# Optimization experiments

Hardware: AMD Instinct MI355X
Metric: run time of the kernel (lower is better)

The kernel has to match this reference:

```python
import jax, jax.numpy as jnp
import numpy as np

# dilation list from _make_freq_dialtion with bins_per_octave=48, n_bins=352,
# max_ratio=9, bin_delta=0: round(48*log2(r)) for r in 2..9
DILATIONS = [48, 76, 96, 111, 124, 135, 144, 152]
B, T, F = 4, 512, 352
CF, HD = 16, 128  # conv_features, hd_conv_features (== dilated_conv_feature)


def _conv(x, w, b, pad, dil=(1, 1)):
    # x: NCHW, w: OIHW; symmetric padding -> matches torch padding=(ph,pw) / 'same' for odd kernels
    y = jax.lax.conv_general_dilated(
        x, w, window_strides=(1, 1),
        padding=[(pad[0], pad[0]), (pad[1], pad[1])],
        rhs_dilation=dil,
        dimension_numbers=("NCHW", "OIHW", "NCHW"))
    return y + b[None, :, None, None]


def _inorm(x, eps=1e-5):
    # torch InstanceNorm2d (affine=False): normalize each (n,c) plane over HxW
    m = jnp.mean(x, axis=(2, 3), keepdims=True)
    v = jnp.var(x, axis=(2, 3), keepdims=True)
    return (x - m) * jax.lax.rsqrt(v + eps)


def setup_inputs() -> dict:
    key = jax.random.key(0)
    ks = jax.random.split(key, 24)

    def w(k, shape, fan_in):
        s = 1.0 / np.sqrt(fan_in)
        return jax.random.uniform(k, shape, jnp.float32, -s, s)

    inp = {}
    inp["cqt"] = jax.random.normal(ks[0], (B, 1, T, F), jnp.float32)
    # 7x7 conv stack
    inp["w0"] = w(ks[1], (CF, 1, 7, 7), 1 * 49);       inp["b0"] = w(ks[2], (CF,), 1 * 49)
    inp["w1"] = w(ks[3], (CF, CF, 7, 7), CF * 49);      inp["b1"] = w(ks[4], (CF,), CF * 49)
    inp["w2"] = w(ks[5], (CF, CF, 7, 7), CF * 49);      inp["b2"] = w(ks[6], (CF,), CF * 49)
    # stacked harmonic dilated convs (1x3), one per dilation
    inp["w_hd"] = w(ks[7], (len(DILATIONS), HD, CF, 1, 3), CF * 3)
    inp["b_hd"] = w(ks[8], (len(DILATIONS), HD), CF * 3)
    # d_cnn
    inp["wd0"] = w(ks[9], (HD, HD, 1, 3), HD * 3);      inp["bd0"] = w(ks[10], (HD,), HD * 3)
    inp["wd1"] = w(ks[11], (HD, HD, 1, 3), HD * 3);     inp["bd1"] = w(ks[12], (HD,), HD * 3)
    inp["wd2"] = w(ks[13], (HD, HD, 5, 1), HD * 5);     inp["bd2"] = w(ks[14], (HD,), HD * 5)
    inp["wd3"] = w(ks[15], (HD, HD, 5, 1), HD * 5);     inp["bd3"] = w(ks[16], (HD,), HD * 5)
    inp["wd4"] = w(ks[17], (HD, HD, 5, 1), HD * 5);     inp["bd4"] = w(ks[18], (HD,), HD * 5)
    return inp


def reference(cqt, w0, b0, w1, b1, w2, b2, w_hd, b_hd,
              wd0, bd0, wd1, bd1, wd2, bd2, wd3, bd3, wd4, bd4):
    x = _inorm(jax.nn.relu(_conv(cqt, w0, b0, (3, 3))))
    x = _inorm(jax.nn.relu(_conv(x, w1, b1, (3, 3))))
    x = _inorm(jax.nn.relu(_conv(x, w2, b2, (3, 3))))
    # multi-branch dilated 1x3 convs, sum-accumulated
    y = None
    for i, d in enumerate(DILATIONS):
        t = _conv(x, w_hd[i], b_hd[i], (0, d), (1, d))
        y = t if y is None else y + t
    # d_cnn
    z = jax.nn.relu(_conv(y, wd0, bd0, (0, 48), (1, 48)))
    z = jax.lax.reduce_window(z, -jnp.inf, jax.lax.max,
                              (1, 1, 1, 4), (1, 1, 1, 4), "VALID")  # MaxPool2d((1,4))
    z = _inorm(z)
    z = _inorm(jax.nn.relu(_conv(z, wd1, bd1, (0, 12), (1, 12))))
    z = _inorm(jax.nn.relu(_conv(z, wd2, bd2, (2, 0))))
    z = _inorm(jax.nn.relu(_conv(z, wd3, bd3, (2, 0))))
    z = _inorm(jax.nn.relu(_conv(z, wd4, bd4, (2, 0))))
    return z  # [B, 128, T, F//4]
```

## Files before the change

### kernel.cpp

```cpp
#include <hip/hip_runtime.h>
#include <hip/hip_bf16.h>

constexpr int B = 4, T = 512, F = 352, CF = 16, HD = 128, F4 = 88;
constexpr int PLANE  = T * F;
constexpr int PLANE4 = T * F4;
constexpr int NDIL = 8;
constexpr int FP = 360;

typedef __attribute__((ext_vector_type(8))) short short8;
typedef __attribute__((ext_vector_type(8))) _Float16 half8;
typedef __attribute__((ext_vector_type(4))) float f32x4;
typedef unsigned short u16;
typedef unsigned long long u64;

#define MFMA(a, b, c)   __builtin_amdgcn_mfma_f32_16x16x32_bf16(a, b, c, 0, 0, 0)
#define MFMA16(a, b, c) __builtin_amdgcn_mfma_f32_16x16x32_f16(a, b, c, 0, 0, 0)

__device__ inline u16 f2bf(float x) {
    unsigned u = __float_as_uint(x);
    return (u16)((u + 0x7fffu + ((u >> 16) & 1u)) >> 16);
}
__device__ inline u16 f2h(float x) {
    _Float16 h = (_Float16)x;
    u16 r; __builtin_memcpy(&r, &h, 2);
    return r;
}

__global__ void prep_hd_pack(const float* __restrict__ w_hd, const float* __restrict__ b_hd,
                             u16* __restrict__ WpP, float* __restrict__ bsum) {
    int tid = blockIdx.x * 256 + threadIdx.x;
    if (tid < HD) {
        float s = 0.f;
        for (int d = 0; d < NDIL; ++d) s += b_hd[d * HD + tid];
        bsum[tid] = s;
    }
    if (tid >= 8 * 9 * 64) return;
    int l = tid & 63, c = (tid >> 6) % 9, og = tid / (9 * 64);
    int cout = og * 16 + (l & 15);
#pragma unroll
    for (int e = 0; e < 8; ++e) {
        int k = c * 32 + ((l >> 4) * 8) + e;
        int tau = k >> 4, ci = k & 15;
        float v = 0.f;
        if (tau == 0) {
            for (int d = 0; d < NDIL; ++d) v += w_hd[((d * HD + cout) * CF + ci) * 3 + 1];
        } else if (tau <= 8) {
            v = w_hd[(((tau - 1) * HD + cout) * CF + ci) * 3 + 0];
        } else if (tau <= 16) {
            v = w_hd[(((tau - 9) * HD + cout) * CF + ci) * 3 + 2];
        }
        WpP[tid * 8 + e] = f2bf(v);
    }
}

__global__ void pack_wd(const float* __restrict__ wsrc, u16* __restrict__ dst,
                        int ntap, int nch) {
    int tid = blockIdx.x * 256 + threadIdx.x;
    if (tid >= 8 * nch * 64) return;
    int l = tid & 63, c = (tid >> 6) % nch, og = tid / (nch * 64);
    int cout = og * 16 + (l & 15);
#pragma unroll
    for (int e = 0; e < 8; ++e) {
        int k = c * 32 + ((l >> 4) * 8) + e;
        int tau = k >> 7, ci = k & 127;
        float v = (tau < ntap) ? wsrc[(cout * HD + ci) * ntap + tau] : 0.f;
        dst[tid * 8 + e] = f2bf(v);
    }
}

__global__ void pack_c7(const float* __restrict__ wsrc, u16* __restrict__ dst) {
    int tid = blockIdx.x * 256 + threadIdx.x;
    if (tid >= 28 * 64) return;
    int l = tid & 63, c = tid >> 6;
    int cout = l & 15, g = l >> 4;
#pragma unroll
    for (int e = 0; e < 8; ++e) {
        int k = c * 32 + g * 8 + e;
        int taup = k >> 4, ci = k & 15;
        int dy = taup >> 3, dx = taup & 7;
        float v = (dx < 7) ? wsrc[((cout * CF + ci) * 7 + dy) * 7 + dx] : 0.f;
        dst[tid * 8 + e] = f2h(v);
    }
}

__global__ __launch_bounds__(256) void conv7x7_c1(
        const float* __restrict__ x, const float* __restrict__ w,
        const float* __restrict__ bias, float* __restrict__ out) {
    int idx = blockIdx.x * 256 + threadIdx.x;
    int f = idx % F;
    int t = (idx / F) % T;
    int n = idx / (F * T);
    float acc[CF];
#pragma unroll
    for (int co = 0; co < CF; ++co) acc[co] = bias[co];
    const float* xp = x + n * PLANE;
    float xv[49];
#pragma unroll
    for (int dy = 0; dy < 7; ++dy) {
        int tt = t + dy - 3;
        bool tok = (unsigned)tt < (unsigned)T;
#pragma unroll
        for (int dx = 0; dx < 7; ++dx) {
            int ff = f + dx - 3;
            xv[dy * 7 + dx] = (tok && (unsigned)ff < (unsigned)F) ? xp[tt * F + ff] : 0.f;
        }
    }
#pragma unroll
    for (int co = 0; co < CF; ++co) {
        const float* wpc = w + co * 49;
#pragma unroll
        for (int k = 0; k < 49; ++k) acc[co] = fmaf(xv[k], wpc[k], acc[co]);
    }
    float* op = out + n * CF * PLANE + t * F + f;
#pragma unroll
    for (int co = 0; co < CF; ++co) op[co * PLANE] = fmaxf(acc[co], 0.f);
}

__global__ __launch_bounds__(256) void conv7_mfma(
        const u16* __restrict__ xb, const u16* __restrict__ wP,
        const float* __restrict__ bias, float* __restrict__ out) {
    const int n = blockIdx.x / T, t = blockIdx.x % T;
    const int l = threadIdx.x & 63, w = threadIdx.x >> 6;
    const int g = l >> 4;
    f32x4 acc[6];
    {
        f32x4 b4 = *(const f32x4*)(bias + g * 4);
#pragma unroll
        for (int i = 0; i < 6; ++i) acc[i] = b4;
    }
    for (int c = 0; c < 28; ++c) {
        int trow = t + (c >> 2) - 3;
        if ((unsigned)trow >= (unsigned)T) continue;
        half8 A = *(const half8*)(wP + c * 512 + l * 8);
        int dx = 2 * (c & 3) + (g >> 1);
        const u16* brow = xb + (size_t)(n * T + trow) * FP * 16;
#pragma unroll
        for (int i = 0; i < 6; ++i) {
            int ft = w + 4 * i;
            if (ft < 22) {
                int fcol = ft * 16 + (l & 15) + dx;
                half8 Bv = *(const half8*)(brow + fcol * 16 + (g & 1) * 8);
                acc[i] = MFMA16(A, Bv, acc[i]);
            }
        }
    }
#pragma unroll
    for (int i = 0; i < 6; ++i) {
        int ft = w + 4 * i;
        if (ft < 22) {
            int f = ft * 16 + (l & 15);
#pragma unroll
            for (int r = 0; r < 4; ++r)
                out[((size_t)(n * CF + g * 4 + r) * T + t) * F + f] = fmaxf(acc[i][r], 0.f);
        }
    }
}

template<int MODE>
__global__ __launch_bounds__(256) void apply_xb(
        const float* __restrict__ xin,
        u16* __restrict__ xb, float* __restrict__ xf32,
        const float* __restrict__ mean, const float* __restrict__ rstd) {
    const int n = blockIdx.x / T, t = blockIdx.x % T;
    const int tid = threadIdx.x;
    float m[CF], r[CF];
#pragma unroll
    for (int ci = 0; ci < CF; ++ci) {
        m[ci] = mean[n * CF + ci];
        r[ci] = rstd[n * CF + ci];
    }
    if (MODE == 0 && tid < 32) {
        int colIdx = tid >> 2;
        int col = colIdx < 3 ? colIdx : 352 + colIdx;
        *(u64*)(xb + ((size_t)(n * T + t) * FP + col) * 16 + (tid & 3) * 4) = 0ULL;
    }
    for (int f = tid; f < F; f += 256) {
        const float* xp = xin + ((size_t)n * CF * T + t) * F + f;
        if (MODE == 0) {
            u64 pk[4];
            u16* ph = (u16*)pk;
#pragma unroll
            for (int ci = 0; ci < CF; ++ci)
                ph[ci] = f2h((xp[ci * PLANE] - m[ci]) * r[ci]);
            u64* dst = (u64*)(xb + ((size_t)(n * T + t) * FP + f + 3) * 16);
#pragma unroll
            for (int q = 0; q < 4; ++q) dst[q] = pk[q];
        } else {
            float* op = xf32 + ((size_t)n * CF * T + t) * F + f;
#pragma unroll
            for (int ci = 0; ci < CF; ++ci)
                op[ci * PLANE] = (xp[ci * PLANE] - m[ci]) * r[ci];
        }
    }
}

__global__ __launch_bounds__(512, 2) void hd_wd0_mfma(
        const float* __restrict__ x1, const u16* __restrict__ WpP,
        const u16* __restrict__ wd0P, const float* __restrict__ bsum,
        const float* __restrict__ bd0, float* __restrict__ zr) {
    extern __shared__ char smem[];
    char* xT = smem;
    char* yT = smem + 672 * 48;
    const int n = blockIdx.x / T, t = blockIdx.x % T;
    const int tid = threadIdx.x, l = tid & 63, wid = tid >> 6;
    const int quad = wid & 1, fq = wid >> 1;
    const int g = l >> 4;

#pragma unroll
    for (int k = 0; k < 4; ++k) {
        int idx = tid + k * 512;
        if (idx < 1920) {
            int row = idx / 6, colb = (idx % 6) * 8;
            int arow = row < 160 ? row : row + 352;
            *(u64*)(xT + arow * 48 + colb) = 0ULL;
        }
    }
#pragma unroll
    for (int k = 0; k < 6; ++k) {
        int idx = tid + k * 512;
        int row = idx >> 5, colb = (idx & 31) * 8;
        int arow = row < 48 ? row : row + 352;
        *(u64*)(yT + arow * 256 + colb) = 0ULL;
    }
    {
        int ci = tid >> 5, fbase = tid & 31;
        const float* xp = x1 + ((size_t)(n * CF + ci) * T + t) * F;
#pragma unroll
        for (int k = 0; k < 11; ++k) {
            int f = fbase + 32 * k;
            *(u16*)(xT + (f + 160) * 48 + ci * 2) = f2bf(xp[f]);
        }
    }
    __syncthreads();

    f32x4 acc[6][4];
#pragma unroll
    for (int og4 = 0; og4 < 4; ++og4) {
        f32x4 b4 = *(const f32x4*)(bsum + (quad * 4 + og4) * 16 + g * 4);
#pragma unroll
        for (int i = 0; i < 6; ++i) acc[i][og4] = b4;
    }
    const int OFFA[9] = {0, -76, -111, -135, -152, 76, 111, 135, 152};
    const int OFFB[9] = {-48, -96, -124, -144, 48, 96, 124, 144, 0};
#pragma unroll
    for (int c = 0; c < 9; ++c) {
        short8 A[4];
#pragma unroll
        for (int og4 = 0; og4 < 4; ++og4)
            A[og4] = *(const short8*)(WpP + ((quad * 4 + og4) * 9 + c) * 512 + l * 8);
        int off = (l >> 5) ? OFFB[c] : OFFA[c];
        int cib = (g & 1) * 16;
#pragma unroll
        for (int i = 0; i < 6; ++i) {
            int ft = fq + 4 * i;
            if (ft < 22) {
                int fr = ft * 16 + (l & 15) + off;
                short8 Bv = *(const short8*)(xT + (fr + 160) * 48 + cib);
#pragma unroll
                for (int og4 = 0; og4 < 4; ++og4) acc[i][og4] = MFMA(A[og4], Bv, acc[i][og4]);
            }
        }
    }
#pragma unroll
    for (int i = 0; i < 6; ++i) {
        int ft = fq + 4 * i;
        if (ft < 22) {
            int f = ft * 16 + (l & 15);
#pragma unroll
            for (int og4 = 0; og4 < 4; ++og4) {
                int cb = ((quad * 4 + og4) * 16 + g * 4) * 2;
                u64 pk = (u64)f2bf(acc[i][og4][0]) | ((u64)f2bf(acc[i][og4][1]) << 16)
                       | ((u64)f2bf(acc[i][og4][2]) << 32) | ((u64)f2bf(acc[i][og4][3]) << 48);
                *(u64*)(yT + (f + 48) * 256 + (cb ^ ((f & 7) << 4))) = pk;
            }
        }
    }
    __syncthreads();

#pragma unroll
    for (int og4 = 0; og4 < 4; ++og4) {
        f32x4 b4 = *(const f32x4*)(bd0 + (quad * 4 + og4) * 16 + g * 4);
#pragma unroll
        for (int i = 0; i < 6; ++i) acc[i][og4] = b4;
    }
#pragma unroll
    for (int c = 0; c < 12; ++c) {
        short8 A[4];
#pragma unroll
        for (int og4 = 0; og4 < 4; ++og4)
            A[og4] = *(const short8*)(wd0P + ((quad * 4 + og4) * 12 + c) * 512 + l * 8);
        int off = (c >> 2) * 48 - 48;
        int cib = (c & 3) * 64 + g * 16;
#pragma unroll
        for (int i = 0; i < 6; ++i) {
            int ft = fq + 4 * i;
            if (ft < 22) {
                int fr = ft * 16 + (l & 15) + off;
                short8 Bv = *(const short8*)(yT + (fr + 48) * 256 + (cib ^ ((fr & 7) << 4)));
#pragma unroll
                for (int og4 = 0; og4 < 4; ++og4) acc[i][og4] = MFMA(A[og4], Bv, acc[i][og4]);
            }
        }
    }
#pragma unroll
    for (int i = 0; i < 6; ++i) {
        int ft = fq + 4 * i;
        if (ft < 22) {
#pragma unroll
            for (int og4 = 0; og4 < 4; ++og4) {
                f32x4 v;
#pragma unroll
                for (int r = 0; r < 4; ++r) {
                    float a = fmaxf(acc[i][og4][r], 0.f);
                    a = fmaxf(a, __shfl_xor(a, 1));
                    a = fmaxf(a, __shfl_xor(a, 2));
                    v[r] = a;
                }
                if ((l & 3) == 0) {
                    int fp = (ft * 16 + (l & 15)) >> 2;
                    int cout0 = (quad * 4 + og4) * 16 + g * 4;
                    *(f32x4*)(zr + ((size_t)(n * T + t) * F4 + fp) * HD + cout0) = v;
                }
            }
        }
    }
}

__global__ __launch_bounds__(256) void wd1_mfma(
        const u16* __restrict__ zb, const u16* __restrict__ wP,
        const float* __restrict__ bias, float* __restrict__ out) {
    __shared__ char lds[128 * 256];
    const int n = blockIdx.x / T, t = blockIdx.x % T;
    const int tid = threadIdx.x, l = tid & 63, w = tid >> 6;
    const int g = l >> 4;
    {
        int cib = (tid & 15) * 16;
        int fi = tid >> 4;
        const u16* src = zb + (size_t)(n * T + t) * F4 * HD;
#pragma unroll
        for (int k = 0; k < 6; ++k) {
            int f = fi + 16 * k;
            if (f < F4) {
                short8 v = *(const short8*)(src + f * HD + (tid & 15) * 8);
                *(short8*)(lds + (f + 16) * 256 + (cib ^ ((f & 7) << 4))) = v;
            }
        }
#pragma unroll
        for (int k = 0; k < 3; ++k) {
            int idx = tid + k * 256;
            if (idx < 640) {
                int row = idx >> 4, slot = idx & 15;
                int arow = row < 16 ? row : row + 88;
                *(u64*)(lds + arow * 256 + slot * 16) = 0ULL;
                *(u64*)(lds + arow * 256 + slot * 16 + 8) = 0ULL;
            }
        }
    }
    __syncthreads();
    f32x4 acc[6][2];
#pragma unroll
    for (int og2 = 0; og2 < 2; ++og2) {
        f32x4 b4 = *(const f32x4*)(bias + (w * 2 + og2) * 16 + g * 4);
#pragma unroll
        for (int i = 0; i < 6; ++i) acc[i][og2] = b4;
    }
#pragma unroll
    for (int c = 0; c < 12; ++c) {
        short8 A0 = *(const short8*)(wP + ((w * 2 + 0) * 12 + c) * 512 + l * 8);
        short8 A1 = *(const short8*)(wP + ((w * 2 + 1) * 12 + c) * 512 + l * 8);
        int off = (c >> 2) * 12 - 12;
        int cib = (c & 3) * 64 + g * 16;
#pragma unroll
        for (int i = 0; i < 6; ++i) {
            int fr = i * 16 + (l & 15) + off;
            short8 Bv = *(const short8*)(lds + (fr + 16) * 256 + (cib ^ ((fr & 7) << 4)));
            acc[i][0] = MFMA(A0, Bv, acc[i][0]);
            acc[i][1] = MFMA(A1, Bv, acc[i][1]);
        }
    }
#pragma unroll
    for (int i = 0; i < 6; ++i) {
        int f = i * 16 + (l & 15);
        if (f < F4) {
#pragma unroll
            for (int og2 = 0; og2 < 2; ++og2) {
                int cout0 = (w * 2 + og2) * 16 + g * 4;
                f32x4 v;
#pragma unroll
                for (int r = 0; r < 4; ++r) v[r] = fmaxf(acc[i][og2][r], 0.f);
                *(f32x4*)(out + ((size_t)(n * T + t) * F4 + f) * HD + cout0) = v;
            }
        }
    }
}

template<bool NCHW_OUT>
__global__ __launch_bounds__(256) void wd5_mfma(
        const u16* __restrict__ zb, const u16* __restrict__ wP,
        const float* __restrict__ bias, float* __restrict__ out) {
    const int n = blockIdx.x / T, t = blockIdx.x % T;
    const int tid = threadIdx.x, l = tid & 63, w = tid >> 6;
    const int g = l >> 4;
    f32x4 acc[6][2];
#pragma unroll
    for (int og2 = 0; og2 < 2; ++og2) {
        f32x4 b4 = *(const f32x4*)(bias + (w * 2 + og2) * 16 + g * 4);
#pragma unroll
        for (int i = 0; i < 6; ++i) acc[i][og2] = b4;
    }
#pragma unroll
    for (int c = 0; c < 20; ++c) {
        int trow = t + (c >> 2) - 2;
        if ((unsigned)trow < (unsigned)T) {
            short8 A0 = *(const short8*)(wP + ((w * 2 + 0) * 20 + c) * 512 + l * 8);
            short8 A1 = *(const short8*)(wP + ((w * 2 + 1) * 20 + c) * 512 + l * 8);
            int cio = (c & 3) * 32 + g * 8;
            const u16* brow = zb + (size_t)(n * T + trow) * F4 * HD;
#pragma unroll
            for (int i = 0; i < 6; ++i) {
                int f = i * 16 + (l & 15);
                short8 Bv = *(const short8*)(brow + f * HD + cio);
                acc[i][0] = MFMA(A0, Bv, acc[i][0]);
                acc[i][1] = MFMA(A1, Bv, acc[i][1]);
            }
        }
    }
#pragma unroll
    for (int i = 0; i < 6; ++i) {
        int f = i * 16 + (l & 15);
        if (f < F4) {
#pragma unroll
            for (int og2 = 0; og2 < 2; ++og2) {
                int cout0 = (w * 2 + og2) * 16 + g * 4;
                if (NCHW_OUT) {
#pragma unroll
                    for (int r = 0; r < 4; ++r)
                        out[((size_t)(n * HD + cout0 + r) * T + t) * F4 + f] =
                            fmaxf(acc[i][og2][r], 0.f);
                } else {
                    f32x4 v;
#pragma unroll
                    for (int r = 0; r < 4; ++r) v[r] = fmaxf(acc[i][og2][r], 0.f);
                    *(f32x4*)(out + ((size_t)(n * T + t) * F4 + f) * HD + cout0) = v;
                }
            }
        }
    }
}

__global__ __launch_bounds__(256) void stats_nhwc(const float* __restrict__ zr,
                                                  float* __restrict__ part) {
    int b = blockIdx.x;
    int n = b >> 6, ch = b & 63;
    int c4 = (threadIdx.x & 31) * 4;
    int rg = threadIdx.x >> 5;
    int row = ch * 8 + rg;
    const float* rp = zr + ((size_t)(n * T + row) * F4) * HD + c4;
    float s0 = 0, s1 = 0, s2 = 0, s3 = 0, q0 = 0, q1 = 0, q2 = 0, q3 = 0;
    for (int f = 0; f < F4; ++f) {
        float4 v = *(const float4*)(rp + f * HD);
        s0 += v.x; s1 += v.y; s2 += v.z; s3 += v.w;
        q0 += v.x * v.x; q1 += v.y * v.y; q2 += v.z * v.z; q3 += v.w * v.w;
    }
    __shared__ float red[8][32][8];
    float* rr = red[rg][threadIdx.x & 31];
    rr[0] = s0; rr[1] = s1; rr[2] = s2; rr[3] = s3;
    rr[4] = q0; rr[5] = q1; rr[6] = q2; rr[7] = q3;
    __syncthreads();
    if (threadIdx.x < 32) {
        float acc[8] = {0, 0, 0, 0, 0, 0, 0, 0};
        for (int j = 0; j < 8; ++j)
            for (int e = 0; e < 8; ++e) acc[e] += red[j][threadIdx.x][e];
        for (int e = 0; e < 4; ++e) {
            part[((size_t)b * HD + threadIdx.x * 4 + e) * 2 + 0] = acc[e];
            part[((size_t)b * HD + threadIdx.x * 4 + e) * 2 + 1] = acc[4 + e];
        }
    }
}

__global__ void finalize_nhwc(const float* __restrict__ part, float* __restrict__ mean,
                              float* __restrict__ rstd) {
    int p = blockIdx.x * blockDim.x + threadIdx.x;
    if (p >= B * HD) return;
    int n = p >> 7, c = p & 127;
    float s = 0, q = 0;
    for (int ch = 0; ch < 64; ++ch) {
        s += part[((size_t)(n * 64 + ch) * HD + c) * 2 + 0];
        q += part[((size_t)(n * 64 + ch) * HD + c) * 2 + 1];
    }
    float m = s / (float)PLANE4;
    mean[p] = m;
    rstd[p] = rsqrtf(q / (float)PLANE4 - m * m + 1e-5f);
}

__global__ __launch_bounds__(256) void apply_nhwc(const float* __restrict__ zr,
                                                  u16* __restrict__ zb,
                                                  const float* __restrict__ mean,
                                                  const float* __restrict__ rstd) {
    int i4 = blockIdx.x * 256 + threadIdx.x;
    int c4 = (i4 & 31) * 4;
    int n = i4 / (T * F4 * 32);
    float4 v = *(const float4*)(zr + (size_t)i4 * 4);
    float4 m = *(const float4*)(mean + n * HD + c4);
    float4 r = *(const float4*)(rstd + n * HD + c4);
    u64 pk = (u64)f2bf((v.x - m.x) * r.x) | ((u64)f2bf((v.y - m.y) * r.y) << 16)
           | ((u64)f2bf((v.z - m.z) * r.z) << 32) | ((u64)f2bf((v.w - m.w) * r.w) << 48);
    *(u64*)(zb + (size_t)i4 * 4) = pk;
}

__global__ __launch_bounds__(256) void inorm_stats(const float* __restrict__ x,
                                                   float* __restrict__ part,
                                                   int plane, int nchunks) {
    int p = blockIdx.x / nchunks, c = blockIdx.x % nchunks;
    int len = plane / nchunks;
    const float4* xp = (const float4*)(x + (size_t)p * plane + (size_t)c * len);
    int n4 = len / 4;
    float s = 0.f, q = 0.f;
    for (int i = threadIdx.x; i < n4; i += 256) {
        float4 v = xp[i];
        s += v.x + v.y + v.z + v.w;
        q += v.x * v.x + v.y * v.y + v.z * v.z + v.w * v.w;
    }
#pragma unroll
    for (int off = 32; off > 0; off >>= 1) {
        s += __shfl_down(s, off);
        q += __shfl_down(q, off);
    }
    __shared__ float ss[4], qq[4];
    int wid = threadIdx.x >> 6;
    if ((threadIdx.x & 63) == 0) { ss[wid] = s; qq[wid] = q; }
    __syncthreads();
    if (threadIdx.x == 0) {
        part[blockIdx.x * 2]     = ss[0] + ss[1] + ss[2] + ss[3];
        part[blockIdx.x * 2 + 1] = qq[0] + qq[1] + qq[2] + qq[3];
    }
}

__global__ void inorm_finalize(const float* __restrict__ part, float* __restrict__ mean,
                               float* __restrict__ rstd, int nplanes, int nchunks,
                               float inv_plane) {
    int p = blockIdx.x * blockDim.x + threadIdx.x;
    if (p >= nplanes) return;
    float s = 0.f, q = 0.f;
    for (int c = 0; c < nchunks; ++c) {
        s += part[(p * nchunks + c) * 2];
        q += part[(p * nchunks + c) * 2 + 1];
    }
    float m = s * inv_plane;
    mean[p] = m;
    rstd[p] = rsqrtf(q * inv_plane - m * m + 1e-5f);
}

template<int PSIZE>
__global__ __launch_bounds__(256) void inorm_apply(const float* __restrict__ in,
                                                   float* __restrict__ out,
                                                   const float* __restrict__ mean,
                                                   const float* __restrict__ rstd) {
    int i4 = blockIdx.x * 256 + threadIdx.x;
    int p = (i4 * 4) / PSIZE;
    float m = mean[p], r = rstd[p];
    float4 v = ((const float4*)in)[i4];
    v.x = (v.x - m) * r; v.y = (v.y - m) * r; v.z = (v.z - m) * r; v.w = (v.w - m) * r;
    ((float4*)out)[i4] = v;
}

extern "C" void kernel_launch(void* const* d_in, const int* in_sizes, int n_in,
                              void* d_out, int out_size, void* d_ws, size_t ws_size,
                              hipStream_t stream) {
    (void)in_sizes; (void)n_in; (void)out_size; (void)ws_size;
    const float* cqt  = (const float*)d_in[0];
    const float* w0   = (const float*)d_in[1];  const float* b0  = (const float*)d_in[2];
    const float* w1   = (const float*)d_in[3];  const float* b1  = (const float*)d_in[4];
    const float* w2   = (const float*)d_in[5];  const float* b2  = (const float*)d_in[6];
    const float* w_hd = (const float*)d_in[7];  const float* bhd = (const float*)d_in[8];
    const float* wd0  = (const float*)d_in[9];  const float* bd0 = (const float*)d_in[10];
    const float* wd1  = (const float*)d_in[11]; const float* bd1 = (const float*)d_in[12];
    const float* wd2  = (const float*)d_in[13]; const float* bd2 = (const float*)d_in[14];
    const float* wd3  = (const float*)d_in[15]; const float* bd3 = (const float*)d_in[16];
    const float* wd4  = (const float*)d_in[17]; const float* bd4 = (const float*)d_in[18];
    float* zr = (float*)d_out;

    float* x1   = (float*)d_ws;
    u16*   zb16 = (u16*)(x1 + (size_t)B * CF * PLANE);
    u16*   xb   = zb16;
    u16*   packW = zb16 + (size_t)23068672 + 2048;
    u16*   WpP  = packW;
    u16*   wd0P = WpP  + 36864;
    u16*   wd1P = wd0P + 49152;
    u16*   wd2P = wd1P + 49152;
    u16*   wd3P = wd2P + 81920;
    u16*   wd4P = wd3P + 81920;
    u16*   c7aP = wd4P + 81920;
    u16*   c7bP = c7aP + 14336;
    float* bsum = (float*)(c7bP + 14336);
    float* part = bsum + 128;
    float* meanb = part + 65536;
    float* rstdb = meanb + 512;

    prep_hd_pack<<<18, 256, 0, stream>>>(w_hd, bhd, WpP, bsum);
    pack_wd<<<24, 256, 0, stream>>>(wd0, wd0P, 3, 12);
    pack_wd<<<24, 256, 0, stream>>>(wd1, wd1P, 3, 12);
    pack_wd<<<40, 256, 0, stream>>>(wd2, wd2P, 5, 20);
    pack_wd<<<40, 256, 0, stream>>>(wd3, wd3P, 5, 20);
    pack_wd<<<40, 256, 0, stream>>>(wd4, wd4P, 5, 20);
    pack_c7<<<7, 256, 0, stream>>>(w1, c7aP);
    pack_c7<<<7, 256, 0, stream>>>(w2, c7bP);

    auto stats_big = [&](float* bin) {
        inorm_stats<<<64 * 8, 256, 0, stream>>>(bin, part, PLANE, 8);
        inorm_finalize<<<1, 64, 0, stream>>>(part, meanb, rstdb, 64, 8, 1.f / PLANE);
    };
    auto norm_nhwc = [&]() {
        stats_nhwc<<<256, 256, 0, stream>>>(zr, part);
        finalize_nhwc<<<2, 256, 0, stream>>>(part, meanb, rstdb);
        apply_nhwc<<<B * T * F4 * HD / 4 / 256, 256, 0, stream>>>(zr, zb16, meanb, rstdb);
    };

    conv7x7_c1<<<B * T * F / 256, 256, 0, stream>>>(cqt, w0, b0, zr);
    stats_big(zr);
    apply_xb<0><<<B * T, 256, 0, stream>>>(zr, xb, nullptr, meanb, rstdb);
    conv7_mfma<<<B * T, 256, 0, stream>>>(xb, c7aP, b1, zr);
    stats_big(zr);
    apply_xb<0><<<B * T, 256, 0, stream>>>(zr, xb, nullptr, meanb, rstdb);
    conv7_mfma<<<B * T, 256, 0, stream>>>(xb, c7bP, b2, zr);
    stats_big(zr);
    apply_xb<1><<<B * T, 256, 0, stream>>>(zr, nullptr, x1, meanb, rstdb);

    hipFuncSetAttribute((const void*)hd_wd0_mfma,
                        hipFuncAttributeMaxDynamicSharedMemorySize, 147456);
    hd_wd0_mfma<<<B * T, 512, 146944, stream>>>(x1, WpP, wd0P, bsum, bd0, zr);
    norm_nhwc();

    wd1_mfma<<<B * T, 256, 0, stream>>>(zb16, wd1P, bd1, zr);
    norm_nhwc();
    wd5_mfma<false><<<B * T, 256, 0, stream>>>(zb16, wd2P, bd2, zr);
    norm_nhwc();
    wd5_mfma<false><<<B * T, 256, 0, stream>>>(zb16, wd3P, bd3, zr);
    norm_nhwc();
    wd5_mfma<true><<<B * T, 256, 0, stream>>>(zb16, wd4P, bd4, zr);

    inorm_stats<<<512 * 4, 256, 0, stream>>>(zr, part, PLANE4, 4);
    inorm_finalize<<<1, 512, 0, stream>>>(part, meanb, rstdb, 512, 4, 1.f / PLANE4);
    inorm_apply<PLANE4><<<512 * PLANE4 / 4 / 256, 256, 0, stream>>>(zr, zr, meanb, rstdb);
}
```

Baseline: 1.192 ms.

## Store intermediates in fp16 NHWC and split hd_wd0 into two half-row blocks

```diff
diff --git a/kernel.cpp b/kernel.cpp
--- a/kernel.cpp
+++ b/kernel.cpp
@@ -5,10 +5,12 @@
 constexpr int PLANE  = T * F;
 constexpr int PLANE4 = T * F4;
 constexpr int NDIL = 8;
-constexpr int FP = 360;
+constexpr int FP  = 360;
+constexpr int XBP = 760, XPAD = 208;
 
 typedef __attribute__((ext_vector_type(8))) short short8;
 typedef __attribute__((ext_vector_type(8))) _Float16 half8;
+typedef __attribute__((ext_vector_type(4))) _Float16 half4;
 typedef __attribute__((ext_vector_type(4))) float f32x4;
 typedef unsigned short u16;
 typedef unsigned long long u64;
@@ -85,7 +87,7 @@
 
 __global__ __launch_bounds__(256) void conv7x7_c1(
         const float* __restrict__ x, const float* __restrict__ w,
-        const float* __restrict__ bias, float* __restrict__ out) {
+        const float* __restrict__ bias, u16* __restrict__ zc) {
     int idx = blockIdx.x * 256 + threadIdx.x;
     int f = idx % F;
     int t = (idx / F) % T;
@@ -111,14 +113,18 @@
 #pragma unroll
         for (int k = 0; k < 49; ++k) acc[co] = fmaf(xv[k], wpc[k], acc[co]);
     }
-    float* op = out + n * CF * PLANE + t * F + f;
-#pragma unroll
-    for (int co = 0; co < CF; ++co) op[co * PLANE] = fmaxf(acc[co], 0.f);
+    u64 pk[4];
+    u16* ph = (u16*)pk;
+#pragma unroll
+    for (int co = 0; co < CF; ++co) ph[co] = f2h(fmaxf(acc[co], 0.f));
+    u64* op = (u64*)(zc + ((size_t)(n * T + t) * F + f) * 16);
+#pragma unroll
+    for (int qd = 0; qd < 4; ++qd) op[qd] = pk[qd];
 }
 
 __global__ __launch_bounds__(256) void conv7_mfma(
         const u16* __restrict__ xb, const u16* __restrict__ wP,
-        const float* __restrict__ bias, float* __restrict__ out) {
+        const float* __restrict__ bias, u16* __restrict__ zc) {
     const int n = blockIdx.x / T, t = blockIdx.x % T;
     const int l = threadIdx.x & 63, w = threadIdx.x >> 6;
     const int g = l >> 4;
@@ -149,99 +155,145 @@
         int ft = w + 4 * i;
         if (ft < 22) {
             int f = ft * 16 + (l & 15);
-#pragma unroll
-            for (int r = 0; r < 4; ++r)
-                out[((size_t)(n * CF + g * 4 + r) * T + t) * F + f] = fmaxf(acc[i][r], 0.f);
-        }
-    }
+            u64 pk;
+            u16* ph = (u16*)&pk;
+#pragma unroll
+            for (int r = 0; r < 4; ++r) ph[r] = f2h(fmaxf(acc[i][r], 0.f));
+            *(u64*)(zc + ((size_t)(n * T + t) * F + f) * 16 + g * 4) = pk;
+        }
+    }
+}
+
+__global__ __launch_bounds__(256) void stats_c16(const u16* __restrict__ zc,
+                                                 float* __restrict__ part) {
+    int b = blockIdx.x;
+    int n = b >> 5, ch = b & 31;
+    int cgrp = threadIdx.x & 3, rt = threadIdx.x >> 2;
+    int l = threadIdx.x & 63, wid = threadIdx.x >> 6;
+    const u16* bp = zc + ((size_t)n * PLANE + ch * 5632) * 16 + cgrp * 4;
+    float s[4] = {0, 0, 0, 0}, q[4] = {0, 0, 0, 0};
+    for (int k = 0; k < 88; ++k) {
+        half4 v = *(const half4*)(bp + (size_t)(rt + 64 * k) * 16);
+#pragma unroll
+        for (int e = 0; e < 4; ++e) { float x = (float)v[e]; s[e] += x; q[e] += x * x; }
+    }
+#pragma unroll
+    for (int off = 32; off >= 4; off >>= 1) {
+#pragma unroll
+        for (int e = 0; e < 4; ++e) { s[e] += __shfl_down(s[e], off); q[e] += __shfl_down(q[e], off); }
+    }
+    __shared__ float red[4][4][8];
+    if (l < 4) {
+#pragma unroll
+        for (int e = 0; e < 4; ++e) { red[wid][l][e] = s[e]; red[wid][l][4 + e] = q[e]; }
+    }
+    __syncthreads();
+    if (threadIdx.x < 4) {
+        float a[8] = {0, 0, 0, 0, 0, 0, 0, 0};
+        for (int w2 = 0; w2 < 4; ++w2)
+            for (int e = 0; e < 8; ++e) a[e] += red[w2][threadIdx.x][e];
+#pragma unroll
+        for (int e = 0; e < 4; ++e) {
+            part[((size_t)b * 16 + threadIdx.x * 4 + e) * 2 + 0] = a[e];
+            part[((size_t)b * 16 + threadIdx.x * 4 + e) * 2 + 1] = a[4 + e];
+        }
+    }
+}
+
+__global__ void finalize_c16(const float* __restrict__ part, float* __restrict__ mean,
+                             float* __restrict__ rstd) {
+    int p = threadIdx.x;
+    if (p >= B * CF) return;
+    int n = p >> 4, c = p & 15;
+    float s = 0, q = 0;
+    for (int ch = 0; ch < 32; ++ch) {
+        s += part[(((size_t)(n * 32 + ch)) * 16 + c) * 2 + 0];
+        q += part[(((size_t)(n * 32 + ch)) * 16 + c) * 2 + 1];
+    }
+    float m = s / (float)PLANE;
+    mean[p] = m;
+    rstd[p] = rsqrtf(q / (float)PLANE - m * m + 1e-5f);
 }
 
 template<int MODE>
-__global__ __launch_bounds__(256) void apply_xb(
-        const float* __restrict__ xin,
-        u16* __restrict__ xb, float* __restrict__ xf32,
+__global__ __launch_bounds__(256) void apply_cnn(
+        const u16* __restrict__ zc, u16* __restrict__ dst,
         const float* __restrict__ mean, const float* __restrict__ rstd) {
     const int n = blockIdx.x / T, t = blockIdx.x % T;
     const int tid = threadIdx.x;
     float m[CF], r[CF];
 #pragma unroll
-    for (int ci = 0; ci < CF; ++ci) {
-        m[ci] = mean[n * CF + ci];
-        r[ci] = rstd[n * CF + ci];
-    }
-    if (MODE == 0 && tid < 32) {
-        int colIdx = tid >> 2;
-        int col = colIdx < 3 ? colIdx : 352 + colIdx;
-        *(u64*)(xb + ((size_t)(n * T + t) * FP + col) * 16 + (tid & 3) * 4) = 0ULL;
-    }
+    for (int ci = 0; ci < CF; ++ci) { m[ci] = mean[n * CF + ci]; r[ci] = rstd[n * CF + ci]; }
+    u16* drow = dst + (size_t)(n * T + t) * (MODE ? XBP : FP) * 16;
+    if (MODE == 0) {
+        if (tid < 32) {
+            int colIdx = tid >> 2;
+            int col = colIdx < 3 ? colIdx : 352 + colIdx;
+            *(u64*)(drow + col * 16 + (tid & 3) * 4) = 0ULL;
+        }
+    } else {
+#pragma unroll
+        for (int k = 0; k < 7; ++k) {
+            int idx = tid + k * 256;
+            if (idx < 1632) {
+                int colIdx = idx >> 2;
+                int col = colIdx < XPAD ? colIdx : colIdx + 352;
+                *(u64*)(drow + col * 16 + (idx & 3) * 4) = 0ULL;
+            }
+        }
+    }
+    const u16* srow = zc + (size_t)(n * T + t) * F * 16;
     for (int f = tid; f < F; f += 256) {
-        const float* xp = xin + ((size_t)n * CF * T + t) * F + f;
-        if (MODE == 0) {
-            u64 pk[4];
-            u16* ph = (u16*)pk;
-#pragma unroll
-            for (int ci = 0; ci < CF; ++ci)
-                ph[ci] = f2h((xp[ci * PLANE] - m[ci]) * r[ci]);
-            u64* dst = (u64*)(xb + ((size_t)(n * T + t) * FP + f + 3) * 16);
-#pragma unroll
-            for (int q = 0; q < 4; ++q) dst[q] = pk[q];
-        } else {
-            float* op = xf32 + ((size_t)n * CF * T + t) * F + f;
-#pragma unroll
-            for (int ci = 0; ci < CF; ++ci)
-                op[ci * PLANE] = (xp[ci * PLANE] - m[ci]) * r[ci];
-        }
-    }
-}
-
-__global__ __launch_bounds__(512, 2) void hd_wd0_mfma(
-        const float* __restrict__ x1, const u16* __restrict__ WpP,
+        const half4* ip = (const half4*)(srow + (size_t)f * 16);
+        u64 ov[4];
+        u16* oh = (u16*)ov;
+#pragma unroll
+        for (int qd = 0; qd < 4; ++qd) {
+            half4 v = ip[qd];
+#pragma unroll
+            for (int e = 0; e < 4; ++e) {
+                int ci = qd * 4 + e;
+                float x = ((float)v[e] - m[ci]) * r[ci];
+                oh[ci] = MODE ? f2bf(x) : f2h(x);
+            }
+        }
+        u64* op = (u64*)(drow + (size_t)(f + (MODE ? XPAD : 3)) * 16);
+#pragma unroll
+        for (int qd = 0; qd < 4; ++qd) op[qd] = ov[qd];
+    }
+}
+
+__global__ __launch_bounds__(512, 4) void hd_wd0_mfma(
+        const u16* __restrict__ xbf, const u16* __restrict__ WpP,
         const u16* __restrict__ wd0P, const float* __restrict__ bsum,
-        const float* __restrict__ bd0, float* __restrict__ zr) {
-    extern __shared__ char smem[];
-    char* xT = smem;
-    char* yT = smem + 672 * 48;
-    const int n = blockIdx.x / T, t = blockIdx.x % T;
+        const float* __restrict__ bd0, u16* __restrict__ zr16) {
+    extern __shared__ char yT[];
+    const int h = blockIdx.x & 1;
+    const int nt = blockIdx.x >> 1;
+    const int n = nt / T, t = nt % T;
     const int tid = threadIdx.x, l = tid & 63, wid = tid >> 6;
     const int quad = wid & 1, fq = wid >> 1;
     const int g = l >> 4;
-
-#pragma unroll
-    for (int k = 0; k < 4; ++k) {
-        int idx = tid + k * 512;
-        if (idx < 1920) {
-            int row = idx / 6, colb = (idx % 6) * 8;
-            int arow = row < 160 ? row : row + 352;
-            *(u64*)(xT + arow * 48 + colb) = 0ULL;
-        }
-    }
-#pragma unroll
-    for (int k = 0; k < 6; ++k) {
-        int idx = tid + k * 512;
-        int row = idx >> 5, colb = (idx & 31) * 8;
-        int arow = row < 48 ? row : row + 352;
-        *(u64*)(yT + arow * 256 + colb) = 0ULL;
-    }
+    const int ybase = h ? 128 : -48;
+    const int comp0 = h ? 128 : 0;
+
     {
-        int ci = tid >> 5, fbase = tid & 31;
-        const float* xp = x1 + ((size_t)(n * CF + ci) * T + t) * F;
-#pragma unroll
-        for (int k = 0; k < 11; ++k) {
-            int f = fbase + 32 * k;
-            *(u16*)(xT + (f + 160) * 48 + ci * 2) = f2bf(xp[f]);
-        }
-    }
-    __syncthreads();
-
-    f32x4 acc[6][4];
+        int base = h ? 224 * 256 : 0;
+#pragma unroll
+        for (int k = 0; k < 3; ++k)
+            *(u64*)(yT + base + (tid + k * 512) * 8) = 0ULL;
+    }
+
+    f32x4 acc[4][4];
 #pragma unroll
     for (int og4 = 0; og4 < 4; ++og4) {
         f32x4 b4 = *(const f32x4*)(bsum + (quad * 4 + og4) * 16 + g * 4);
 #pragma unroll
-        for (int i = 0; i < 6; ++i) acc[i][og4] = b4;
+        for (int i = 0; i < 4; ++i) acc[i][og4] = b4;
     }
     const int OFFA[9] = {0, -76, -111, -135, -152, 76, 111, 135, 152};
     const int OFFB[9] = {-48, -96, -124, -144, 48, 96, 124, 144, 0};
+    const u16* xrow = xbf + (size_t)(n * T + t) * XBP * 16;
 #pragma unroll
     for (int c = 0; c < 9; ++c) {
         short8 A[4];
@@ -249,29 +301,28 @@
         for (int og4 = 0; og4 < 4; ++og4)
             A[og4] = *(const short8*)(WpP + ((quad * 4 + og4) * 9 + c) * 512 + l * 8);
         int off = (l >> 5) ? OFFB[c] : OFFA[c];
-        int cib = (g & 1) * 16;
-#pragma unroll
-        for (int i = 0; i < 6; ++i) {
+#pragma unroll
+        for (int i = 0; i < 4; ++i) {
             int ft = fq + 4 * i;
-            if (ft < 22) {
-                int fr = ft * 16 + (l & 15) + off;
-                short8 Bv = *(const short8*)(xT + (fr + 160) * 48 + cib);
+            if (ft < 14) {
+                int f = comp0 + ft * 16 + (l & 15);
+                short8 Bv = *(const short8*)(xrow + (size_t)(f + off + XPAD) * 16 + (g & 1) * 8);
 #pragma unroll
                 for (int og4 = 0; og4 < 4; ++og4) acc[i][og4] = MFMA(A[og4], Bv, acc[i][og4]);
             }
         }
     }
 #pragma unroll
-    for (int i = 0; i < 6; ++i) {
+    for (int i = 0; i < 4; ++i) {
         int ft = fq + 4 * i;
-        if (ft < 22) {
-            int f = ft * 16 + (l & 15);
+        if (ft < 14) {
+            int lrow = (comp0 + ft * 16 + (l & 15)) - ybase;
 #pragma unroll
             for (int og4 = 0; og4 < 4; ++og4) {
                 int cb = ((quad * 4 + og4) * 16 + g * 4) * 2;
                 u64 pk = (u64)f2bf(acc[i][og4][0]) | ((u64)f2bf(acc[i][og4][1]) << 16)
                        | ((u64)f2bf(acc[i][og4][2]) << 32) | ((u64)f2bf(acc[i][og4][3]) << 48);
-                *(u64*)(yT + (f + 48) * 256 + (cb ^ ((f & 7) << 4))) = pk;
+                *(u64*)(yT + lrow * 256 + (cb ^ ((lrow & 7) << 4))) = pk;
             }
         }
     }
@@ -281,7 +332,7 @@
     for (int og4 = 0; og4 < 4; ++og4) {
         f32x4 b4 = *(const f32x4*)(bd0 + (quad * 4 + og4) * 16 + g * 4);
 #pragma unroll
-        for (int i = 0; i < 6; ++i) acc[i][og4] = b4;
+        for (int i = 0; i < 3; ++i) acc[i][og4] = b4;
     }
 #pragma unroll
     for (int c = 0; c < 12; ++c) {
@@ -292,34 +343,35 @@
         int off = (c >> 2) * 48 - 48;
         int cib = (c & 3) * 64 + g * 16;
 #pragma unroll
-        for (int i = 0; i < 6; ++i) {
+        for (int i = 0; i < 3; ++i) {
             int ft = fq + 4 * i;
-            if (ft < 22) {
-                int fr = ft * 16 + (l & 15) + off;
-                short8 Bv = *(const short8*)(yT + (fr + 48) * 256 + (cib ^ ((fr & 7) << 4)));
+            if (ft < 11) {
+                int lr = (h * 176 + ft * 16 + (l & 15)) + off - ybase;
+                short8 Bv = *(const short8*)(yT + lr * 256 + (cib ^ ((lr & 7) << 4)));
 #pragma unroll
                 for (int og4 = 0; og4 < 4; ++og4) acc[i][og4] = MFMA(A[og4], Bv, acc[i][og4]);
             }
         }
     }
 #pragma unroll
-    for (int i = 0; i < 6; ++i) {
+    for (int i = 0; i < 3; ++i) {
         int ft = fq + 4 * i;
-        if (ft < 22) {
+        if (ft < 11) {
 #pragma unroll
             for (int og4 = 0; og4 < 4; ++og4) {
-                f32x4 v;
+                u64 pk;
+                u16* ph = (u16*)&pk;
 #pragma unroll
                 for (int r = 0; r < 4; ++r) {
                     float a = fmaxf(acc[i][og4][r], 0.f);
                     a = fmaxf(a, __shfl_xor(a, 1));
                     a = fmaxf(a, __shfl_xor(a, 2));
-                    v[r] = a;
+                    ph[r] = f2h(a);
                 }
                 if ((l & 3) == 0) {
-                    int fp = (ft * 16 + (l & 15)) >> 2;
+                    int fp = (h * 176 + ft * 16 + (l & 15)) >> 2;
                     int cout0 = (quad * 4 + og4) * 16 + g * 4;
-                    *(f32x4*)(zr + ((size_t)(n * T + t) * F4 + fp) * HD + cout0) = v;
+                    *(u64*)(zr16 + ((size_t)(n * T + t) * F4 + fp) * HD + cout0) = pk;
                 }
             }
         }
@@ -328,7 +380,7 @@
 
 __global__ __launch_bounds__(256) void wd1_mfma(
         const u16* __restrict__ zb, const u16* __restrict__ wP,
-        const float* __restrict__ bias, float* __restrict__ out) {
+        const float* __restrict__ bias, u16* __restrict__ out) {
     __shared__ char lds[128 * 256];
     const int n = blockIdx.x / T, t = blockIdx.x % T;
     const int tid = threadIdx.x, l = tid & 63, w = tid >> 6;
@@ -385,10 +437,11 @@
 #pragma unroll
             for (int og2 = 0; og2 < 2; ++og2) {
                 int cout0 = (w * 2 + og2) * 16 + g * 4;
-                f32x4 v;
-#pragma unroll
-                for (int r = 0; r < 4; ++r) v[r] = fmaxf(acc[i][og2][r], 0.f);
-                *(f32x4*)(out + ((size_t)(n * T + t) * F4 + f) * HD + cout0) = v;
+                u64 pk;
+                u16* ph = (u16*)&pk;
+#pragma unroll
+                for (int r = 0; r < 4; ++r) ph[r] = f2h(fmaxf(acc[i][og2][r], 0.f));
+                *(u64*)(out + ((size_t)(n * T + t) * F4 + f) * HD + cout0) = pk;
             }
         }
     }
@@ -397,7 +450,7 @@
 template<bool NCHW_OUT>
 __global__ __launch_bounds__(256) void wd5_mfma(
         const u16* __restrict__ zb, const u16* __restrict__ wP,
-        const float* __restrict__ bias, float* __restrict__ out) {
+        const float* __restrict__ bias, u16* __restrict__ out) {
     const int n = blockIdx.x / T, t = blockIdx.x % T;
     const int tid = threadIdx.x, l = tid & 63, w = tid >> 6;
     const int g = l >> 4;
@@ -436,31 +489,33 @@
 #pragma unroll
                     for (int r = 0; r < 4; ++r)
                         out[((size_t)(n * HD + cout0 + r) * T + t) * F4 + f] =
-                            fmaxf(acc[i][og2][r], 0.f);
+                            f2h(fmaxf(acc[i][og2][r], 0.f));
                 } else {
-                    f32x4 v;
-#pragma unroll
-                    for (int r = 0; r < 4; ++r) v[r] = fmaxf(acc[i][og2][r], 0.f);
-                    *(f32x4*)(out + ((size_t)(n * T + t) * F4 + f) * HD + cout0) = v;
+                    u64 pk;
+                    u16* ph = (u16*)&pk;
+#pragma unroll
+                    for (int r = 0; r < 4; ++r) ph[r] = f2h(fmaxf(acc[i][og2][r], 0.f));
+                    *(u64*)(out + ((size_t)(n * T + t) * F4 + f) * HD + cout0) = pk;
                 }
             }
         }
     }
 }
 
-__global__ __launch_bounds__(256) void stats_nhwc(const float* __restrict__ zr,
+__global__ __launch_bounds__(256) void stats_c128(const u16* __restrict__ zr16,
                                                   float* __restrict__ part) {
     int b = blockIdx.x;
     int n = b >> 6, ch = b & 63;
     int c4 = (threadIdx.x & 31) * 4;
     int rg = threadIdx.x >> 5;
     int row = ch * 8 + rg;
-    const float* rp = zr + ((size_t)(n * T + row) * F4) * HD + c4;
+    const u16* rp = zr16 + ((size_t)(n * T + row) * F4) * HD + c4;
     float s0 = 0, s1 = 0, s2 = 0, s3 = 0, q0 = 0, q1 = 0, q2 = 0, q3 = 0;
     for (int f = 0; f < F4; ++f) {
-        float4 v = *(const float4*)(rp + f * HD);
-        s0 += v.x; s1 += v.y; s2 += v.z; s3 += v.w;
-        q0 += v.x * v.x; q1 += v.y * v.y; q2 += v.z * v.z; q3 += v.w * v.w;
+        half4 v = *(const half4*)(rp + (size_t)f * HD);
+        float x0 = (float)v[0], x1 = (float)v[1], x2 = (float)v[2], x3 = (float)v[3];
+        s0 += x0; s1 += x1; s2 += x2; s3 += x3;
+        q0 += x0 * x0; q1 += x1 * x1; q2 += x2 * x2; q3 += x3 * x3;
     }
     __shared__ float red[8][32][8];
     float* rr = red[rg][threadIdx.x & 31];
@@ -493,33 +548,32 @@
     rstd[p] = rsqrtf(q / (float)PLANE4 - m * m + 1e-5f);
 }
 
-__global__ __launch_bounds__(256) void apply_nhwc(const float* __restrict__ zr,
-                                                  u16* __restrict__ zb,
-                                                  const float* __restrict__ mean,
-                                                  const float* __restrict__ rstd) {
-    int i4 = blockIdx.x * 256 + threadIdx.x;
-    int c4 = (i4 & 31) * 4;
-    int n = i4 / (T * F4 * 32);
-    float4 v = *(const float4*)(zr + (size_t)i4 * 4);
-    float4 m = *(const float4*)(mean + n * HD + c4);
-    float4 r = *(const float4*)(rstd + n * HD + c4);
-    u64 pk = (u64)f2bf((v.x - m.x) * r.x) | ((u64)f2bf((v.y - m.y) * r.y) << 16)
-           | ((u64)f2bf((v.z - m.z) * r.z) << 32) | ((u64)f2bf((v.w - m.w) * r.w) << 48);
-    *(u64*)(zb + (size_t)i4 * 4) = pk;
-}
-
-__global__ __launch_bounds__(256) void inorm_stats(const float* __restrict__ x,
-                                                   float* __restrict__ part,
-                                                   int plane, int nchunks) {
-    int p = blockIdx.x / nchunks, c = blockIdx.x % nchunks;
-    int len = plane / nchunks;
-    const float4* xp = (const float4*)(x + (size_t)p * plane + (size_t)c * len);
-    int n4 = len / 4;
+__global__ __launch_bounds__(256) void apply_z(const u16* __restrict__ zr16,
+                                               u16* __restrict__ zb,
+                                               const float* __restrict__ mean,
+                                               const float* __restrict__ rstd) {
+    int i8 = blockIdx.x * 256 + threadIdx.x;
+    int c8 = (i8 & 15) * 8;
+    int n = i8 / (T * F4 * 16);
+    half8 hv = *(const half8*)(zr16 + (size_t)i8 * 8);
+    const float* mp = mean + n * HD + c8;
+    const float* rp = rstd + n * HD + c8;
+    short8 o;
+#pragma unroll
+    for (int e = 0; e < 8; ++e)
+        o[e] = (short)f2bf(((float)hv[e] - mp[e]) * rp[e]);
+    *(short8*)(zb + (size_t)i8 * 8) = o;
+}
+
+__global__ __launch_bounds__(256) void stats_nchw16(const u16* __restrict__ x,
+                                                    float* __restrict__ part) {
+    int p = blockIdx.x >> 2, c = blockIdx.x & 3;
+    const u16* xp = x + (size_t)p * PLANE4 + c * 11264;
     float s = 0.f, q = 0.f;
-    for (int i = threadIdx.x; i < n4; i += 256) {
-        float4 v = xp[i];
-        s += v.x + v.y + v.z + v.w;
-        q += v.x * v.x + v.y * v.y + v.z * v.z + v.w * v.w;
+    for (int i = threadIdx.x; i < 1408; i += 256) {
+        half8 v = *(const half8*)(xp + (size_t)i * 8);
+#pragma unroll
+        for (int e = 0; e < 8; ++e) { float xx = (float)v[e]; s += xx; q += xx * xx; }
     }
 #pragma unroll
     for (int off = 32; off > 0; off >>= 1) {
@@ -551,17 +605,21 @@
     rstd[p] = rsqrtf(q * inv_plane - m * m + 1e-5f);
 }
 
-template<int PSIZE>
-__global__ __launch_bounds__(256) void inorm_apply(const float* __restrict__ in,
-                                                   float* __restrict__ out,
-                                                   const float* __restrict__ mean,
-                                                   const float* __restrict__ rstd) {
-    int i4 = blockIdx.x * 256 + threadIdx.x;
-    int p = (i4 * 4) / PSIZE;
+__global__ __launch_bounds__(256) void apply_nchw16(const u16* __restrict__ x,
+                                                    float* __restrict__ out,
+                                                    const float* __restrict__ mean,
+                                                    const float* __restrict__ rstd) {
+    int i8 = blockIdx.x * 256 + threadIdx.x;
+    int p = (int)(((long long)i8 * 8) / PLANE4);
     float m = mean[p], r = rstd[p];
-    float4 v = ((const float4*)in)[i4];
-    v.x = (v.x - m) * r; v.y = (v.y - m) * r; v.z = (v.z - m) * r; v.w = (v.w - m) * r;
-    ((float4*)out)[i4] = v;
+    half8 v = *(const half8*)(x + (size_t)i8 * 8);
+    f32x4 o0, o1;
+#pragma unroll
+    for (int e = 0; e < 4; ++e) o0[e] = ((float)v[e] - m) * r;
+#pragma unroll
+    for (int e = 0; e < 4; ++e) o1[e] = ((float)v[4 + e] - m) * r;
+    *(f32x4*)(out + (size_t)i8 * 8) = o0;
+    *(f32x4*)(out + (size_t)i8 * 8 + 4) = o1;
 }
 
 extern "C" void kernel_launch(void* const* d_in, const int* in_sizes, int n_in,
@@ -578,24 +636,28 @@
     const float* wd2  = (const float*)d_in[13]; const float* bd2 = (const float*)d_in[14];
     const float* wd3  = (const float*)d_in[15]; const float* bd3 = (const float*)d_in[16];
     const float* wd4  = (const float*)d_in[17]; const float* bd4 = (const float*)d_in[18];
-    float* zr = (float*)d_out;
-
-    float* x1   = (float*)d_ws;
-    u16*   zb16 = (u16*)(x1 + (size_t)B * CF * PLANE);
-    u16*   xb   = zb16;
-    u16*   packW = zb16 + (size_t)23068672 + 2048;
-    u16*   WpP  = packW;
-    u16*   wd0P = WpP  + 36864;
-    u16*   wd1P = wd0P + 49152;
-    u16*   wd2P = wd1P + 49152;
-    u16*   wd3P = wd2P + 81920;
-    u16*   wd4P = wd3P + 81920;
-    u16*   c7aP = wd4P + 81920;
-    u16*   c7bP = c7aP + 14336;
-    float* bsum = (float*)(c7bP + 14336);
-    float* part = bsum + 128;
+
+    u16* xbf  = (u16*)d_ws;
+    u16* zz16 = xbf;
+    u16* zb16 = xbf + 24903680;
+    u16* WpP  = zb16 + 23068672;
+    u16* wd0P = WpP  + 36864;
+    u16* wd1P = wd0P + 49152;
+    u16* wd2P = wd1P + 49152;
+    u16* wd3P = wd2P + 81920;
+    u16* wd4P = wd3P + 81920;
+    u16* c7aP = wd4P + 81920;
+    u16* c7bP = c7aP + 14336;
+    float* bsum  = (float*)(c7bP + 14336);
+    float* part  = bsum + 128;
     float* meanb = part + 65536;
     float* rstdb = meanb + 512;
+
+    u16* zdo  = (u16*)d_out;
+    u16* zc   = zdo;
+    u16* xb   = zdo + 11534336;
+    u16* zr16 = zdo;
+    float* outf = (float*)d_out;
 
     prep_hd_pack<<<18, 256, 0, stream>>>(w_hd, bhd, WpP, bsum);
     pack_wd<<<24, 256, 0, stream>>>(wd0, wd0P, 3, 12);
@@ -606,40 +668,39 @@
     pack_c7<<<7, 256, 0, stream>>>(w1, c7aP);
     pack_c7<<<7, 256, 0, stream>>>(w2, c7bP);
 
-    auto stats_big = [&](float* bin) {
-        inorm_stats<<<64 * 8, 256, 0, stream>>>(bin, part, PLANE, 8);
-        inorm_finalize<<<1, 64, 0, stream>>>(part, meanb, rstdb, 64, 8, 1.f / PLANE);
+    auto norm_cnn16 = [&](int mode) {
+        stats_c16<<<B * 32, 256, 0, stream>>>(zc, part);
+        finalize_c16<<<1, 64, 0, stream>>>(part, meanb, rstdb);
+        if (mode == 0) apply_cnn<0><<<B * T, 256, 0, stream>>>(zc, xb, meanb, rstdb);
+        else           apply_cnn<1><<<B * T, 256, 0, stream>>>(zc, xbf, meanb, rstdb);
     };
-    auto norm_nhwc = [&]() {
-        stats_nhwc<<<256, 256, 0, stream>>>(zr, part);
+    auto norm_z = [&]() {
+        stats_c128<<<256, 256, 0, stream>>>(zr16, part);
         finalize_nhwc<<<2, 256, 0, stream>>>(part, meanb, rstdb);
-        apply_nhwc<<<B * T * F4 * HD / 4 / 256, 256, 0, stream>>>(zr, zb16, meanb, rstdb);
+        apply_z<<<11264, 256, 0, stream>>>(zr16, zb16, meanb, rstdb);
     };
 
-    conv7x7_c1<<<B * T * F / 256, 256, 0, stream>>>(cqt, w0, b0, zr);
-    stats_big(zr);
-    apply_xb<0><<<B * T, 256, 0, stream>>>(zr, xb, nullptr, meanb, rstdb);
-    conv7_mfma<<<B * T, 256, 0, stream>>>(xb, c7aP, b1, zr);
-    stats_big(zr);
-    apply_xb<0><<<B * T, 256, 0, stream>>>(zr, xb, nullptr, meanb, rstdb);
-    conv7_mfma<<<B * T, 256, 0, stream>>>(xb, c7bP, b2, zr);
-    stats_big(zr);
-    apply_xb<1><<<B * T, 256, 0, stream>>>(zr, nullptr, x1, meanb, rstdb);
+    conv7x7_c1<<<B * T * F / 256, 256, 0, stream>>>(cqt, w0, b0, zc);
+    norm_cnn16(0);
+    conv7_mfma<<<B * T, 256, 0, stream>>>(xb, c7aP, b1, zc);
+    norm_cnn16(0);
+    conv7_mfma<<<B * T, 256, 0, stream>>>(xb, c7bP, b2, zc);
+    norm_cnn16(1);
 
     hipFuncSetAttribute((const void*)hd_wd0_mfma,
-                        hipFuncAttributeMaxDynamicSharedMemorySize, 147456);
-    hd_wd0_mfma<<<B * T, 512, 146944, stream>>>(x1, WpP, wd0P, bsum, bd0, zr);
-    norm_nhwc();
-
-    wd1_mfma<<<B * T, 256, 0, stream>>>(zb16, wd1P, bd1, zr);
-    norm_nhwc();
-    wd5_mfma<false><<<B * T, 256, 0, stream>>>(zb16, wd2P, bd2, zr);
-    norm_nhwc();
-    wd5_mfma<false><<<B * T, 256, 0, stream>>>(zb16, wd3P, bd3, zr);
-    norm_nhwc();
-    wd5_mfma<true><<<B * T, 256, 0, stream>>>(zb16, wd4P, bd4, zr);
-
-    inorm_stats<<<512 * 4, 256, 0, stream>>>(zr, part, PLANE4, 4);
-    inorm_finalize<<<1, 512, 0, stream>>>(part, meanb, rstdb, 512, 4, 1.f / PLANE4);
-    inorm_apply<PLANE4><<<512 * PLANE4 / 4 / 256, 256, 0, stream>>>(zr, zr, meanb, rstdb);
-}
+                        hipFuncAttributeMaxDynamicSharedMemorySize, 69632);
+    hd_wd0_mfma<<<B * T * 2, 512, 69632, stream>>>(xbf, WpP, wd0P, bsum, bd0, zr16);
+    norm_z();
+
+    wd1_mfma<<<B * T, 256, 0, stream>>>(zb16, wd1P, bd1, zr16);
+    norm_z();
+    wd5_mfma<false><<<B * T, 256, 0, stream>>>(zb16, wd2P, bd2, zr16);
+    norm_z();
+    wd5_mfma<false><<<B * T, 256, 0, stream>>>(zb16, wd3P, bd3, zr16);
+    norm_z();
+    wd5_mfma<true><<<B * T, 256, 0, stream>>>(zb16, wd4P, bd4, zz16);
+
+    stats_nchw16<<<B * HD * 4, 256, 0, stream>>>(zz16, part);
+    inorm_finalize<<<2, 256, 0, stream>>>(part, meanb, rstdb, 512, 4, 1.f / PLANE4);
+    apply_nchw16<<<11264, 256, 0, stream>>>(zz16, outf, meanb, rstdb);
+}
```

New measurement: 1.133 ms. 1.05x faster.
